# Kernel optimization log

Hardware: AMD Instinct MI355X
Metric: run time of the kernel (lower is better)

Reference implementation:

```python
import jax, jax.numpy as jnp
import numpy as np


def setup_inputs() -> dict:
    key = jax.random.key(0)
    ks = jax.random.split(key, 6)
    b, t, k, h = 2, 2048, 256, 8
    s = 1.0 / np.sqrt(k)
    return {
        "x": jax.random.normal(ks[0], (b, t, k), dtype=jnp.float32),
        "Wq": jax.random.normal(ks[1], (k, k * h), dtype=jnp.float32) * s,
        "Wk": jax.random.normal(ks[2], (k, k * h), dtype=jnp.float32) * s,
        "Wv": jax.random.normal(ks[3], (k, k * h), dtype=jnp.float32) * s,
        "Wu": jax.random.normal(ks[4], (k * h, k), dtype=jnp.float32) * (1.0 / np.sqrt(k * h)),
        "bu": jnp.zeros((k,), dtype=jnp.float32),
    }


def reference(x, Wq, Wk, Wv, Wu, bu):
    b, t, k = x.shape
    h = Wq.shape[1] // k
    scale = k ** (-0.25)
    # projections -> [b, t, h, k] -> [b, h, t, k]
    q = (x @ Wq).reshape(b, t, h, k).transpose(0, 2, 1, 3) * scale
    kk = (x @ Wk).reshape(b, t, h, k).transpose(0, 2, 1, 3) * scale
    v = (x @ Wv).reshape(b, t, h, k).transpose(0, 2, 1, 3)
    dot = jnp.einsum('bhqk,bhsk->bhqs', q, kk)  # [b,h,t,t]
    attn = jax.nn.softmax(dot, axis=-1)
    out = jnp.einsum('bhqs,bhsk->bhqk', attn, v)  # [b,h,t,k]
    out = out.transpose(0, 2, 1, 3).reshape(b, t, h * k)
    return out @ Wu + bu
```

## Files before the change

kernel.cpp:

```cpp
#include <hip/hip_runtime.h>

using bf16x8   = __bf16 __attribute__((ext_vector_type(8)));
using floatx4  = float __attribute__((ext_vector_type(4)));
using floatx16 = float __attribute__((ext_vector_type(16)));

static __device__ __forceinline__ unsigned short f2b(float x) {
  unsigned u = __builtin_bit_cast(unsigned, x);
  u = (u + 0x7fffu + ((u >> 16) & 1u)) >> 16;
  return (unsigned short)u;
}

static __device__ __forceinline__ void gl_lds16(const unsigned short* g, unsigned short* l) {
  __builtin_amdgcn_global_load_lds((const __attribute__((address_space(1))) void*)g,
                                   (__attribute__((address_space(3))) void*)l, 16, 0, 0);
}

__global__ __launch_bounds__(256) void prep_kernel(const float* __restrict__ x,
                                                   const float* __restrict__ Wq,
                                                   const float* __restrict__ Wk,
                                                   const float* __restrict__ Wv,
                                                   const float* __restrict__ Wu,
                                                   unsigned short* __restrict__ xb,
                                                   unsigned short* __restrict__ wqkt,
                                                   unsigned short* __restrict__ wvt,
                                                   unsigned short* __restrict__ wut) {
  int bx = blockIdx.x;
  if (bx < 1024) {
    int i = (bx * 256 + threadIdx.x) * 4;
    float4 v = *(const float4*)(x + i);
    unsigned long long p = (unsigned long long)f2b(v.x) |
                           ((unsigned long long)f2b(v.y) << 16) |
                           ((unsigned long long)f2b(v.z) << 32) |
                           ((unsigned long long)f2b(v.w) << 48);
    *(unsigned long long*)(xb + i) = p;
    return;
  }
  __shared__ unsigned short T[64][65];
  const float* src;
  unsigned short* dst;
  int R, C, tile;
  if (bx < 1152)      { src = Wq; dst = wqkt;          R = 256;  C = 2048; tile = bx - 1024; }
  else if (bx < 1280) { src = Wk; dst = wqkt + 524288; R = 256;  C = 2048; tile = bx - 1152; }
  else if (bx < 1408) { src = Wv; dst = wvt;           R = 256;  C = 2048; tile = bx - 1280; }
  else                { src = Wu; dst = wut;           R = 2048; C = 256;  tile = bx - 1408; }
  int ctiles = C >> 6;
  int cx = tile % ctiles, ry = tile / ctiles;
  int r0 = ry * 64, c0 = cx * 64;
  int t = threadIdx.x;
#pragma unroll
  for (int i = 0; i < 16; ++i) {
    int idx = i * 256 + t;
    int r = idx >> 6, c = idx & 63;
    T[r][c] = f2b(src[(size_t)(r0 + r) * C + c0 + c]);
  }
  __syncthreads();
#pragma unroll
  for (int i = 0; i < 16; ++i) {
    int idx = i * 256 + t;
    int c = idx >> 6, r = idx & 63;
    dst[(size_t)(c0 + c) * R + r0 + r] = T[r][c];
  }
}

__global__ __launch_bounds__(256) void proj_kernel(const unsigned short* __restrict__ A,
                                                   const unsigned short* __restrict__ Bt,
                                                   unsigned short* __restrict__ qkb,
                                                   unsigned short* __restrict__ vtb) {
  __shared__ __align__(16) unsigned short SMEM[128 * 136];
  const int Kt = 256;
  int tid = threadIdx.x, lane = tid & 63, w = tid >> 6;
  int m16 = lane & 15, quad = lane >> 4;
  int wr = w & 1, wc = w >> 1;
  int m0 = blockIdx.y * 128, n0 = blockIdx.x * 128;
  int srow0 = w * 32 + (lane >> 2);
  int schunk = (lane & 3) ^ ((lane >> 2) & 3);
  floatx4 acc[4][4] = {};
#pragma unroll
  for (int j = 0; j < 2; ++j) {
    int r = srow0 + j * 16;
    gl_lds16(A + (size_t)(m0 + r) * Kt + schunk * 8, &SMEM[(w * 32 + j * 16) * 32]);
    gl_lds16(Bt + (size_t)(n0 + r) * Kt + schunk * 8, &SMEM[4096 + (w * 32 + j * 16) * 32]);
  }
  for (int k0 = 0; k0 < Kt; k0 += 32) {
    int cur = (k0 >> 5) & 1;
    unsigned short* As = SMEM + cur * 8192;
    unsigned short* Bs = As + 4096;
    __syncthreads();
    if (k0 + 32 < Kt) {
      unsigned short* Ad = SMEM + (1 - cur) * 8192;
      unsigned short* Bd = Ad + 4096;
#pragma unroll
      for (int j = 0; j < 2; ++j) {
        int r = srow0 + j * 16;
        gl_lds16(A + (size_t)(m0 + r) * Kt + k0 + 32 + schunk * 8, Ad + (w * 32 + j * 16) * 32);
        gl_lds16(Bt + (size_t)(n0 + r) * Kt + k0 + 32 + schunk * 8, Bd + (w * 32 + j * 16) * 32);
      }
    }
    int sw = (quad ^ (m16 & 3)) * 8;
    bf16x8 af[4], bfr[4];
#pragma unroll
    for (int i = 0; i < 4; ++i) {
      af[i]  = *(const bf16x8*)(&As[(wr * 64 + i * 16 + m16) * 32 + sw]);
      bfr[i] = *(const bf16x8*)(&Bs[(wc * 64 + i * 16 + m16) * 32 + sw]);
    }
#pragma unroll
    for (int i = 0; i < 4; ++i)
#pragma unroll
      for (int jn = 0; jn < 4; ++jn)
        acc[i][jn] = __builtin_amdgcn_mfma_f32_16x16x32_bf16(af[i], bfr[jn], acc[i][jn], 0, 0, 0);
  }
  if (n0 < 4096) {
    float qscale = (n0 < 2048) ? 0.0625f : 1.0f;
#pragma unroll
    for (int i = 0; i < 4; ++i)
#pragma unroll
      for (int jn = 0; jn < 4; ++jn)
#pragma unroll
        for (int r = 0; r < 4; ++r) {
          int m = m0 + wr * 64 + i * 16 + quad * 4 + r;
          int n = n0 + wc * 64 + jn * 16 + m16;
          qkb[(size_t)m * 4096 + n] = f2b(acc[i][jn][r] * qscale);
        }
  } else {
    __syncthreads();
    unsigned short* Vt = SMEM;
#pragma unroll
    for (int i = 0; i < 4; ++i)
#pragma unroll
      for (int jn = 0; jn < 4; ++jn)
#pragma unroll
        for (int r = 0; r < 4; ++r) {
          int nn = wc * 64 + jn * 16 + m16;
          int mm = wr * 64 + i * 16 + quad * 4 + r;
          Vt[nn * 136 + mm] = f2b(acc[i][jn][r]);
        }
    __syncthreads();
    int bb = m0 >> 11, t0 = m0 & 2047;
#pragma unroll
    for (int i2 = 0; i2 < 8; ++i2) {
      int idx = i2 * 256 + tid;
      int nn = idx >> 4;
      int mc = (idx & 15) * 8;
      uint4 v = *(const uint4*)(&Vt[nn * 136 + mc]);
      *(uint4*)(&vtb[((size_t)(bb * 2048 + n0 - 4096 + nn)) * 2048 + t0 + mc]) = v;
    }
  }
}

__global__ __launch_bounds__(256) void out_kernel(const unsigned short* __restrict__ A,
                                                  const unsigned short* __restrict__ Bt,
                                                  float* __restrict__ Cout,
                                                  const float* __restrict__ bias) {
  __shared__ __align__(16) unsigned short SMEM[32768];
  const int Kt = 2048;
  int tid = threadIdx.x, lane = tid & 63, w = tid >> 6;
  int m16 = lane & 15, quad = lane >> 4;
  int m0 = blockIdx.y * 64, n0 = blockIdx.x * 64;
  int srow_i = lane >> 4;
  int spos = lane & 15;
  int rsw = m16 & 7;
  floatx4 acc[4] = {};
#pragma unroll
  for (int j = 0; j < 4; ++j) {
    int r = w * 16 + j * 4 + srow_i;
    gl_lds16(A + (size_t)(m0 + r) * Kt + ((spos ^ (r & 7)) * 8), &SMEM[(w * 16 + j * 4) * 128]);
    gl_lds16(Bt + (size_t)(n0 + r) * Kt + ((spos ^ (r & 7)) * 8), &SMEM[8192 + (w * 16 + j * 4) * 128]);
  }
  for (int k0 = 0; k0 < Kt; k0 += 128) {
    int cur = (k0 >> 7) & 1;
    unsigned short* As = SMEM + cur * 16384;
    unsigned short* Bs = As + 8192;
    __syncthreads();
    if (k0 + 128 < Kt) {
      unsigned short* Ad = SMEM + (1 - cur) * 16384;
      unsigned short* Bd = Ad + 8192;
#pragma unroll
      for (int j = 0; j < 4; ++j) {
        int r = w * 16 + j * 4 + srow_i;
        gl_lds16(A + (size_t)(m0 + r) * Kt + k0 + 128 + ((spos ^ (r & 7)) * 8),
                 Ad + (w * 16 + j * 4) * 128);
        gl_lds16(Bt + (size_t)(n0 + r) * Kt + k0 + 128 + ((spos ^ (r & 7)) * 8),
                 Bd + (w * 16 + j * 4) * 128);
      }
    }
    bf16x8 af[4];
#pragma unroll
    for (int kk = 0; kk < 4; ++kk)
      af[kk] = *(const bf16x8*)(&As[(w * 16 + m16) * 128 + (((kk * 4 + quad) ^ rsw) * 8)]);
#pragma unroll
    for (int nt = 0; nt < 4; ++nt)
#pragma unroll
      for (int kk = 0; kk < 4; ++kk) {
        bf16x8 bfv = *(const bf16x8*)(&Bs[(nt * 16 + m16) * 128 + (((kk * 4 + quad) ^ rsw) * 8)]);
        acc[nt] = __builtin_amdgcn_mfma_f32_16x16x32_bf16(af[kk], bfv, acc[nt], 0, 0, 0);
      }
  }
#pragma unroll
  for (int nt = 0; nt < 4; ++nt)
#pragma unroll
    for (int r = 0; r < 4; ++r) {
      int m = m0 + w * 16 + quad * 4 + r;
      int n = n0 + nt * 16 + m16;
      Cout[(size_t)m * 256 + n] = acc[nt][r] + bias[n];
    }
}

__global__ __launch_bounds__(512, 2) void attn_kernel(const unsigned short* __restrict__ qk,
                                                      const unsigned short* __restrict__ vt,
                                                      unsigned short* __restrict__ ao) {
  __shared__ __align__(16) unsigned short Ks[2][64 * 256];
  __shared__ __align__(16) unsigned short Vs[2][256 * 64];
  __shared__ __align__(16) unsigned short Pb[4][32 * 72];
  int tid = threadIdx.x, lane = tid & 63, w = tid >> 6;
  int c32 = lane & 31, hi = lane >> 5;
  int qg = w & 3, u = w >> 2;
  int id = blockIdx.x;
  int xcd = id & 7, j = id >> 3;
  int bh = xcd + 8 * (j & 1);
  int q0 = (j >> 1) * 128;
  int b = bh >> 3, h = bh & 7;

  bf16x8 qf[16];
  const unsigned short* qrow =
      qk + (size_t)(b * 2048 + q0 + qg * 32 + c32) * 4096 + h * 256 + hi * 8;
#pragma unroll
  for (int kk = 0; kk < 16; ++kk) qf[kk] = *(const bf16x8*)(qrow + kk * 16);

  bf16x8 onesf;
#pragma unroll
  for (int i = 0; i < 8; ++i) onesf[i] = (__bf16)1.0f;

  floatx16 O[4] = {};
  floatx16 l = {};

  const unsigned short* kbase = qk + (size_t)b * 2048 * 4096 + 2048 + h * 256;
  const unsigned short* vbase = vt + (size_t)bh * 256 * 2048;
  unsigned short* pq = &Pb[qg][0];

  int krow_i = lane >> 5, kpos = lane & 31;
  int vrow_i = lane >> 3, vpos = lane & 7;
  int ksw = c32 & 7;

#pragma unroll
  for (int i = 0; i < 4; ++i) {
    int kr = i * 2 + krow_i;
    gl_lds16(kbase + (size_t)(w * 8 + kr) * 4096 + ((kpos ^ (kr & 7)) * 8),
             &Ks[0][(w * 8 + i * 2) * 256]);
    int vr = i * 8 + vrow_i;
    gl_lds16(vbase + (size_t)(w * 32 + vr) * 2048 + ((vpos ^ vrow_i) * 8),
             &Vs[0][(w * 32 + i * 8) * 64]);
  }

  for (int st = 0; st < 32; ++st) {
    int cur = st & 1;
    __syncthreads();

    floatx16 s = {};
    const unsigned short* krl = &Ks[cur][(u * 32 + c32) * 256];
#pragma unroll
    for (int kk = 0; kk < 16; ++kk) {
      bf16x8 kf = *(const bf16x8*)(krl + (((kk * 2 + hi) ^ ksw) * 8));
      s = __builtin_amdgcn_mfma_f32_32x32x16_bf16(qf[kk], kf, s, 0, 0, 0);
    }
#pragma unroll
    for (int i = 0; i < 16; ++i) {
      float p = __expf(s[i]);
      int q = (i & 3) + 8 * (i >> 2) + 4 * hi;
      pq[q * 72 + u * 32 + c32] = f2b(p);
    }
    __syncthreads();

    if (st < 31) {
      int s0 = (st + 1) * 64;
      unsigned short* kdst = &Ks[1 - cur][0];
      unsigned short* vdst = &Vs[1 - cur][0];
#pragma unroll
      for (int i = 0; i < 4; ++i) {
        int kr = i * 2 + krow_i;
        gl_lds16(kbase + (size_t)(s0 + w * 8 + kr) * 4096 + ((kpos ^ (kr & 7)) * 8),
                 kdst + (w * 8 + i * 2) * 256);
        int vr = i * 8 + vrow_i;
        gl_lds16(vbase + (size_t)(w * 32 + vr) * 2048 + s0 + ((vpos ^ vrow_i) * 8),
                 vdst + (w * 32 + i * 8) * 64);
      }
    }

    bf16x8 paf[4];
#pragma unroll
    for (int f = 0; f < 4; ++f) paf[f] = *(const bf16x8*)(pq + c32 * 72 + f * 16 + hi * 8);
#pragma unroll
    for (int f = 0; f < 4; ++f)
      l = __builtin_amdgcn_mfma_f32_32x32x16_bf16(paf[f], onesf, l, 0, 0, 0);
#pragma unroll
    for (int dt = 0; dt < 4; ++dt) {
      const unsigned short* vrl = &Vs[cur][(u * 128 + dt * 32 + c32) * 64];
#pragma unroll
      for (int f = 0; f < 4; ++f) {
        bf16x8 vf = *(const bf16x8*)(vrl + (((f * 2 + hi) ^ ksw) * 8));
        O[dt] = __builtin_amdgcn_mfma_f32_32x32x16_bf16(paf[f], vf, O[dt], 0, 0, 0);
      }
    }
  }
  float inv[16];
#pragma unroll
  for (int i = 0; i < 16; ++i) inv[i] = 1.0f / l[i];
#pragma unroll
  for (int dt = 0; dt < 4; ++dt)
#pragma unroll
    for (int i = 0; i < 16; ++i) {
      int q = (i & 3) + 8 * (i >> 2) + 4 * hi;
      ao[(size_t)(b * 2048 + q0 + qg * 32 + q) * 2048 + h * 256 + u * 128 + dt * 32 + c32] =
          f2b(O[dt][i] * inv[i]);
    }
}

extern "C" void kernel_launch(void* const* d_in, const int* in_sizes, int n_in,
                              void* d_out, int out_size, void* d_ws, size_t ws_size,
                              hipStream_t stream) {
  const float* x  = (const float*)d_in[0];
  const float* Wq = (const float*)d_in[1];
  const float* Wk = (const float*)d_in[2];
  const float* Wv = (const float*)d_in[3];
  const float* Wu = (const float*)d_in[4];
  const float* bu = (const float*)d_in[5];

  unsigned short* xb   = (unsigned short*)d_ws;
  unsigned short* wqkt = xb + 1048576;
  unsigned short* wvt  = wqkt + 1048576;
  unsigned short* wut  = wvt + 524288;
  unsigned short* qkb  = wut + 524288;
  unsigned short* vtb  = qkb + 16777216;
  unsigned short* aob  = vtb + 8388608;

  prep_kernel<<<1536, 256, 0, stream>>>(x, Wq, Wk, Wv, Wu, xb, wqkt, wvt, wut);
  proj_kernel<<<dim3(48, 32), 256, 0, stream>>>(xb, wqkt, qkb, vtb);
  attn_kernel<<<256, 512, 0, stream>>>(qkb, vtb, aob);
  out_kernel<<<dim3(4, 64), 256, 0, stream>>>(aob, wut, (float*)d_out, bu);
}
```

Measured before the change: 192.1 us.

## Stage QK projection stores through LDS and split-K the output GEMM

The Q/K projection epilogue now writes its tile into shared memory and then emits coalesced 16-byte row stores, instead of scattered 2-byte global stores. The output projection is split along K into two halves via a third grid dimension, doubling the block count from 256 to 512. The two halves combine with float atomicAdd into an output buffer zeroed by a memset, with the bias added only by the first half. This adds a memset launch plus atomic traffic, and makes the float summation order nondeterministic.

Result: slower. 196.7 us (+2.4%).

```diff
diff --git a/kernel.cpp b/kernel.cpp
--- a/kernel.cpp
+++ b/kernel.cpp
@@ -109,6 +109,8 @@
       for (int jn = 0; jn < 4; ++jn)
         acc[i][jn] = __builtin_amdgcn_mfma_f32_16x16x32_bf16(af[i], bfr[jn], acc[i][jn], 0, 0, 0);
   }
+  __syncthreads();
+  unsigned short* T = SMEM;
   if (n0 < 4096) {
     float qscale = (n0 < 2048) ? 0.0625f : 1.0f;
 #pragma unroll
@@ -117,13 +119,20 @@
       for (int jn = 0; jn < 4; ++jn)
 #pragma unroll
         for (int r = 0; r < 4; ++r) {
-          int m = m0 + wr * 64 + i * 16 + quad * 4 + r;
-          int n = n0 + wc * 64 + jn * 16 + m16;
-          qkb[(size_t)m * 4096 + n] = f2b(acc[i][jn][r] * qscale);
+          int mm = wr * 64 + i * 16 + quad * 4 + r;
+          int nn = wc * 64 + jn * 16 + m16;
+          T[mm * 136 + nn] = f2b(acc[i][jn][r] * qscale);
         }
+    __syncthreads();
+#pragma unroll
+    for (int i2 = 0; i2 < 8; ++i2) {
+      int idx = i2 * 256 + tid;
+      int row = idx >> 4;
+      int mc = (idx & 15) * 8;
+      uint4 v = *(const uint4*)(&T[row * 136 + mc]);
+      *(uint4*)(&qkb[(size_t)(m0 + row) * 4096 + n0 + mc]) = v;
+    }
   } else {
-    __syncthreads();
-    unsigned short* Vt = SMEM;
 #pragma unroll
     for (int i = 0; i < 4; ++i)
 #pragma unroll
@@ -132,7 +141,7 @@
         for (int r = 0; r < 4; ++r) {
           int nn = wc * 64 + jn * 16 + m16;
           int mm = wr * 64 + i * 16 + quad * 4 + r;
-          Vt[nn * 136 + mm] = f2b(acc[i][jn][r]);
+          T[nn * 136 + mm] = f2b(acc[i][jn][r]);
         }
     __syncthreads();
     int bb = m0 >> 11, t0 = m0 & 2047;
@@ -141,7 +150,7 @@
       int idx = i2 * 256 + tid;
       int nn = idx >> 4;
       int mc = (idx & 15) * 8;
-      uint4 v = *(const uint4*)(&Vt[nn * 136 + mc]);
+      uint4 v = *(const uint4*)(&T[nn * 136 + mc]);
       *(uint4*)(&vtb[((size_t)(bb * 2048 + n0 - 4096 + nn)) * 2048 + t0 + mc]) = v;
     }
   }
@@ -156,6 +165,7 @@
   int tid = threadIdx.x, lane = tid & 63, w = tid >> 6;
   int m16 = lane & 15, quad = lane >> 4;
   int m0 = blockIdx.y * 64, n0 = blockIdx.x * 64;
+  int kb = blockIdx.z * 1024;
   int srow_i = lane >> 4;
   int spos = lane & 15;
   int rsw = m16 & 7;
@@ -163,15 +173,15 @@
 #pragma unroll
   for (int j = 0; j < 4; ++j) {
     int r = w * 16 + j * 4 + srow_i;
-    gl_lds16(A + (size_t)(m0 + r) * Kt + ((spos ^ (r & 7)) * 8), &SMEM[(w * 16 + j * 4) * 128]);
-    gl_lds16(Bt + (size_t)(n0 + r) * Kt + ((spos ^ (r & 7)) * 8), &SMEM[8192 + (w * 16 + j * 4) * 128]);
-  }
-  for (int k0 = 0; k0 < Kt; k0 += 128) {
-    int cur = (k0 >> 7) & 1;
+    gl_lds16(A + (size_t)(m0 + r) * Kt + kb + ((spos ^ (r & 7)) * 8), &SMEM[(w * 16 + j * 4) * 128]);
+    gl_lds16(Bt + (size_t)(n0 + r) * Kt + kb + ((spos ^ (r & 7)) * 8), &SMEM[8192 + (w * 16 + j * 4) * 128]);
+  }
+  for (int k0 = kb; k0 < kb + 1024; k0 += 128) {
+    int cur = ((k0 - kb) >> 7) & 1;
     unsigned short* As = SMEM + cur * 16384;
     unsigned short* Bs = As + 8192;
     __syncthreads();
-    if (k0 + 128 < Kt) {
+    if (k0 + 128 < kb + 1024) {
       unsigned short* Ad = SMEM + (1 - cur) * 16384;
       unsigned short* Bd = Ad + 8192;
 #pragma unroll
@@ -201,7 +211,8 @@
     for (int r = 0; r < 4; ++r) {
       int m = m0 + w * 16 + quad * 4 + r;
       int n = n0 + nt * 16 + m16;
-      Cout[(size_t)m * 256 + n] = acc[nt][r] + bias[n];
+      float v = acc[nt][r] + (blockIdx.z == 0 ? bias[n] : 0.0f);
+      atomicAdd(&Cout[(size_t)m * 256 + n], v);
     }
 }
 
@@ -335,5 +346,6 @@
   prep_kernel<<<1536, 256, 0, stream>>>(x, Wq, Wk, Wv, Wu, xb, wqkt, wvt, wut);
   proj_kernel<<<dim3(48, 32), 256, 0, stream>>>(xb, wqkt, qkb, vtb);
   attn_kernel<<<256, 512, 0, stream>>>(qkb, vtb, aob);
-  out_kernel<<<dim3(4, 64), 256, 0, stream>>>(aob, wut, (float*)d_out, bu);
-}
+  hipMemsetAsync(d_out, 0, (size_t)out_size * sizeof(float), stream);
+  out_kernel<<<dim3(4, 64, 2), 256, 0, stream>>>(aob, wut, (float*)d_out, bu);
+}
```
